# Optimization experiments

Measured on AMD Instinct MI355X. Metric: run time of the kernel, lower is better.

## Reference

```python
import jax, jax.numpy as jnp
import numpy as np

B, C, HID, H, W_ = 16, 2048, 256, 32, 32

def setup_inputs() -> dict:
    key = jax.random.key(0)
    k1, k2, k3 = jax.random.split(key, 3)
    return {
        "query_features": jax.random.normal(k1, (B, C, H, W_), dtype=jnp.float32),
        "prompt_features": jax.random.normal(k2, (B, C, H, W_), dtype=jnp.float32),
        "W": jax.random.normal(k3, (HID, C), dtype=jnp.float32) * 0.02,
        "b": jnp.zeros((HID,), dtype=jnp.float32),
    }

def reference(query_features, prompt_features, W, b):
    Bq, Cc, Hh, Ww = query_features.shape
    HW = Hh * Ww
    # 1x1 conv == channel matmul
    Q = jnp.einsum('oc,bchw->bohw', W, query_features) + b[None, :, None, None]
    K = jnp.einsum('oc,bchw->bohw', W, prompt_features) + b[None, :, None, None]
    Qf = Q.reshape(Bq, -1, HW)          # (b, hid, HW1)
    Kf = K.reshape(Bq, -1, HW)          # (b, hid, HW2)
    Vf = prompt_features.reshape(Bq, Cc, HW)  # (b, C, HW2)
    scores = jnp.einsum('bcq,bck->bqk', Qf, Kf)   # (b, HW1, HW2)
    A = jax.nn.softmax(scores, axis=-1)
    aligned = jnp.einsum('bqk,bck->bcq', A, Vf).reshape(Bq, Cc, Hh, Ww)
    # fusion_policy == 'cat'
    return jnp.concatenate([query_features, aligned], axis=1)
```

## Files before the change

### kernel.cpp

```cpp
#include <hip/hip_runtime.h>

#define NB   16
#define NC   2048
#define NHID 256
#define NHW  1024

using half4_t  = __attribute__((ext_vector_type(4))) _Float16;
using half8_t  = __attribute__((ext_vector_type(8))) _Float16;
using float4_t = __attribute__((ext_vector_type(4))) float;

#define OUT_BATCH_BYTES ((size_t)(4096u * 1024u) * 4u)

__device__ __forceinline__ void async_load16(const void* g, void* l) {
    __builtin_amdgcn_global_load_lds((__attribute__((address_space(1))) void*)g,
                                     (__attribute__((address_space(3))) void*)l, 16, 0, 0);
}

__device__ __forceinline__ void stage_async(const _Float16* __restrict__ src, size_t stride_h,
                                            _Float16* __restrict__ lds, int t) {
    #pragma unroll
    for (int i = 0; i < 4; ++i) {
        const int o   = i * 4096 + t * 16;
        const int row = o >> 7;
        const int s   = ((o >> 4) & 7) ^ (row & 7);
        const _Float16* g = src + (size_t)row * stride_h + s * 8;
        async_load16(g, (char*)lds + o);
    }
}

__device__ __forceinline__ half8_t frag_read(const _Float16* __restrict__ lds, int row, int kk, int quad) {
    const int s = (kk * 4 + quad) ^ (row & 7);
    return *(const half8_t*)((const char*)lds + row * 128 + s * 16);
}

#define ACC_INIT(acc) \
    _Pragma("unroll") for (int i_ = 0; i_ < 4; ++i_) \
    _Pragma("unroll") for (int j_ = 0; j_ < 4; ++j_) \
    _Pragma("unroll") for (int r_ = 0; r_ < 4; ++r_) acc[i_][j_][r_] = 0.f;

__device__ __forceinline__ void gemm_f16(const _Float16* __restrict__ A, size_t lda,
                                         const _Float16* __restrict__ B, size_t ldb,
                                         int K, _Float16* __restrict__ As, _Float16* __restrict__ Bs,
                                         float4_t acc[4][4]) {
    const int t = threadIdx.x;
    const int l = t & 63, quad = l >> 4, l15 = l & 15;
    const int w = t >> 6;
    const int wr = (w >> 1) * 64, wc = (w & 1) * 64;
    for (int k0 = 0; k0 < K; k0 += 64) {
        stage_async(A + k0, lda, As, t);
        stage_async(B + k0, ldb, Bs, t);
        __syncthreads();
        #pragma unroll
        for (int kk = 0; kk < 2; ++kk) {
            half8_t af[4], bf[4];
            #pragma unroll
            for (int i = 0; i < 4; ++i) af[i] = frag_read(As, wr + i * 16 + l15, kk, quad);
            #pragma unroll
            for (int j = 0; j < 4; ++j) bf[j] = frag_read(Bs, wc + j * 16 + l15, kk, quad);
            #pragma unroll
            for (int i = 0; i < 4; ++i)
                #pragma unroll
                for (int j = 0; j < 4; ++j)
                    acc[i][j] = __builtin_amdgcn_mfma_f32_16x16x32_f16(af[i], bf[j], acc[i][j], 0, 0, 0);
        }
        __syncthreads();
    }
}

__global__ __launch_bounds__(256) void prep_kernel(
    const float* __restrict__ qf, const float* __restrict__ pf,
    _Float16* __restrict__ qT, float* __restrict__ out) {
    __shared__ _Float16 tile[64][72];
    const int z = blockIdx.z, which = z >> 4, b = z & 15;
    const int c0 = blockIdx.y * 64, h0 = blockIdx.x * 64;
    const float* X = (which ? pf : qf) + (size_t)b * NC * NHW;
    _Float16* T = which ? (_Float16*)((char*)out + (size_t)b * OUT_BATCH_BYTES + (4u << 20))
                        : (qT + (size_t)b * NHW * NC);
    const int t = threadIdx.x;
    const int row = t >> 2, seg = t & 3;
    const float* src = X + (size_t)(c0 + row) * NHW + h0 + seg * 16;
    float4 v[4];
    #pragma unroll
    for (int i = 0; i < 4; ++i) v[i] = *(const float4*)(src + i * 4);
    half8_t h[2];
    #pragma unroll
    for (int i = 0; i < 2; ++i) {
        #pragma unroll
        for (int e = 0; e < 4; ++e) {
            h[i][e]     = (_Float16)((&v[2 * i].x)[e]);
            h[i][4 + e] = (_Float16)((&v[2 * i + 1].x)[e]);
        }
        *(half8_t*)&tile[row][seg * 16 + i * 8] = h[i];
    }
    if (which) {
        _Float16* vd = (_Float16*)((char*)out + (size_t)b * OUT_BATCH_BYTES)
                       + (size_t)(c0 + row) * NHW + h0 + seg * 16;
        *(half8_t*)vd = h[0];
        *(half8_t*)(vd + 8) = h[1];
    }
    __syncthreads();
    const int hr = t >> 2;
    half8_t o[2];
    #pragma unroll
    for (int i = 0; i < 2; ++i)
        #pragma unroll
        for (int e = 0; e < 8; ++e) o[i][e] = tile[seg * 16 + i * 8 + e][hr];
    _Float16* od = T + (size_t)(h0 + hr) * NC + c0 + seg * 16;
    *(half8_t*)od = o[0];
    *(half8_t*)(od + 8) = o[1];
}

__global__ __launch_bounds__(256) void wcvt_kernel(const float* __restrict__ W, _Float16* __restrict__ W16) {
    const int idx = (blockIdx.x * 256 + threadIdx.x) * 8;
    float4 a = *(const float4*)(W + idx);
    float4 c = *(const float4*)(W + idx + 4);
    half8_t h;
    h[0] = (_Float16)a.x; h[1] = (_Float16)a.y; h[2] = (_Float16)a.z; h[3] = (_Float16)a.w;
    h[4] = (_Float16)c.x; h[5] = (_Float16)c.y; h[6] = (_Float16)c.z; h[7] = (_Float16)c.w;
    *(half8_t*)(W16 + idx) = h;
}

__global__ __launch_bounds__(256) void proj16_kernel(
    const _Float16* __restrict__ qT, const float* __restrict__ out_scratch,
    const _Float16* __restrict__ W16, const float* __restrict__ bias,
    _Float16* __restrict__ Q16, _Float16* __restrict__ K16) {
    __shared__ __attribute__((aligned(16))) _Float16 As[8192];
    __shared__ __attribute__((aligned(16))) _Float16 Bs[8192];
    const int z = blockIdx.z, which = z >> 4, b = z & 15;
    const _Float16* X = which
        ? (const _Float16*)((const char*)out_scratch + (size_t)b * OUT_BATCH_BYTES + (4u << 20))
        : (qT + (size_t)b * NHW * NC);
    _Float16* O = (which ? K16 : Q16) + (size_t)b * NHW * NHID;
    const int m0 = blockIdx.y * 128, n0 = blockIdx.x * 128;
    float4_t acc[4][4];
    ACC_INIT(acc)
    gemm_f16(X + (size_t)m0 * NC, NC, W16 + (size_t)n0 * NC, NC, NC, As, Bs, acc);
    const int t = threadIdx.x, l = t & 63, quad = l >> 4, l15 = l & 15, w = t >> 6;
    const int wr = (w >> 1) * 64, wc = (w & 1) * 64;
    #pragma unroll
    for (int j = 0; j < 4; ++j) {
        const float bv = bias[n0 + wc + j * 16 + l15];
        #pragma unroll
        for (int i = 0; i < 4; ++i)
            #pragma unroll
            for (int r = 0; r < 4; ++r) {
                int hw  = m0 + wr + i * 16 + quad * 4 + r;
                int hid = n0 + wc + j * 16 + l15;
                O[(size_t)hw * NHID + hid] = (_Float16)(acc[i][j][r] + bv);
            }
    }
}

__global__ __launch_bounds__(256) void scores16_kernel(
    const _Float16* __restrict__ Q16, const _Float16* __restrict__ K16, float* __restrict__ S) {
    __shared__ __attribute__((aligned(16))) _Float16 As[8192];
    __shared__ __attribute__((aligned(16))) _Float16 Bs[8192];
    const int b = blockIdx.z;
    const int m0 = blockIdx.y * 128, n0 = blockIdx.x * 128;
    float* Sb = S + (size_t)b * NHW * NHW;
    float4_t acc[4][4];
    ACC_INIT(acc)
    gemm_f16(Q16 + (size_t)b * NHW * NHID + (size_t)m0 * NHID, NHID,
             K16 + (size_t)b * NHW * NHID + (size_t)n0 * NHID, NHID, NHID, As, Bs, acc);
    const int t = threadIdx.x, l = t & 63, quad = l >> 4, l15 = l & 15, w = t >> 6;
    const int wr = (w >> 1) * 64, wc = (w & 1) * 64;
    #pragma unroll
    for (int i = 0; i < 4; ++i)
        #pragma unroll
        for (int j = 0; j < 4; ++j)
            #pragma unroll
            for (int r = 0; r < 4; ++r) {
                int q1 = m0 + wr + i * 16 + quad * 4 + r;
                int q2 = n0 + wc + j * 16 + l15;
                Sb[(size_t)q1 * NHW + q2] = acc[i][j][r];
            }
}

__global__ __launch_bounds__(256) void softmax_kernel(float* __restrict__ S) {
    const int t = threadIdx.x, wave = t >> 6, lane = t & 63;
    float* row = S + ((size_t)blockIdx.x * 4 + wave) * NHW;
    float4 v[4];
    float mx = -1e30f;
    #pragma unroll
    for (int j = 0; j < 4; ++j) {
        v[j] = *(const float4*)(row + (lane << 2) + (j << 8));
        mx = fmaxf(mx, fmaxf(fmaxf(v[j].x, v[j].y), fmaxf(v[j].z, v[j].w)));
    }
    #pragma unroll
    for (int off = 32; off >= 1; off >>= 1) mx = fmaxf(mx, __shfl_xor(mx, off, 64));
    float s = 0.f;
    #pragma unroll
    for (int j = 0; j < 4; ++j) {
        v[j].x = __expf(v[j].x - mx); v[j].y = __expf(v[j].y - mx);
        v[j].z = __expf(v[j].z - mx); v[j].w = __expf(v[j].w - mx);
        s += v[j].x + v[j].y + v[j].z + v[j].w;
    }
    #pragma unroll
    for (int off = 32; off >= 1; off >>= 1) s += __shfl_xor(s, off, 64);
    const float inv = 1.0f / s;
    __syncthreads();
    _Float16* o = (_Float16*)row;
    #pragma unroll
    for (int j = 0; j < 4; ++j) {
        half4_t h;
        h[0] = (_Float16)(v[j].x * inv); h[1] = (_Float16)(v[j].y * inv);
        h[2] = (_Float16)(v[j].z * inv); h[3] = (_Float16)(v[j].w * inv);
        *(half4_t*)(o + (lane << 2) + (j << 8)) = h;
    }
}

__global__ __launch_bounds__(256) void av16_kernel(
    const float* __restrict__ S, float* __restrict__ out) {
    __shared__ __attribute__((aligned(16))) _Float16 As[8192];
    __shared__ __attribute__((aligned(16))) _Float16 Bs[8192];
    const int b = blockIdx.z;
    const _Float16* Vb  = (const _Float16*)((const char*)out + (size_t)b * OUT_BATCH_BYTES);
    const _Float16* A16 = (const _Float16*)(S + (size_t)b * NHW * NHW);
    float* Ob = out + (size_t)b * (2 * NC) * NHW + (size_t)NC * NHW;
    const int m0 = blockIdx.y * 128;
    const int n0 = blockIdx.x * 128;
    float4_t acc[4][4];
    ACC_INIT(acc)
    gemm_f16(Vb + (size_t)m0 * NHW, NHW, A16 + (size_t)n0 * 2048, 2048, NHW, As, Bs, acc);
    const int t = threadIdx.x, l = t & 63, quad = l >> 4, l15 = l & 15, w = t >> 6;
    const int wr = (w >> 1) * 64, wc = (w & 1) * 64;
    #pragma unroll
    for (int i = 0; i < 4; ++i)
        #pragma unroll
        for (int j = 0; j < 4; ++j)
            #pragma unroll
            for (int r = 0; r < 4; ++r) {
                int c = m0 + wr + i * 16 + quad * 4 + r;
                int q = n0 + wc + j * 16 + l15;
                Ob[(size_t)c * NHW + q] = acc[i][j][r];
            }
}

__global__ __launch_bounds__(256) void copy_kernel(const uint4* __restrict__ qf,
                                                   uint4* __restrict__ out) {
    int idx = blockIdx.x * 256 + threadIdx.x;
    int b = idx >> 19;
    int r = idx & 0x7FFFF;
    out[((size_t)b << 20) + r] = qf[idx];
}

extern "C" void kernel_launch(void* const* d_in, const int* in_sizes, int n_in,
                              void* d_out, int out_size, void* d_ws, size_t ws_size,
                              hipStream_t stream) {
    const float* qf   = (const float*)d_in[0];
    const float* pf   = (const float*)d_in[1];
    const float* Wm   = (const float*)d_in[2];
    const float* bias = (const float*)d_in[3];
    float* out = (float*)d_out;

    _Float16* qT  = (_Float16*)d_ws;
    float*    S   = (float*)d_ws;
    _Float16* Q16 = (_Float16*)((char*)d_ws + ((size_t)64 << 20));
    _Float16* K16 = (_Float16*)((char*)d_ws + ((size_t)72 << 20));
    _Float16* W16 = (_Float16*)((char*)out + ((size_t)8 << 20));

    prep_kernel<<<dim3(16, 32, 32), 256, 0, stream>>>(qf, pf, qT, out);
    wcvt_kernel<<<256, 256, 0, stream>>>(Wm, W16);
    proj16_kernel<<<dim3(2, 8, 32), 256, 0, stream>>>(qT, out, W16, bias, Q16, K16);
    scores16_kernel<<<dim3(8, 8, 16), 256, 0, stream>>>(Q16, K16, S);
    softmax_kernel<<<NB * 256, 256, 0, stream>>>(S);
    av16_kernel<<<dim3(8, 16, 16), 256, 0, stream>>>(S, out);
    copy_kernel<<<32768, 256, 0, stream>>>((const uint4*)qf, (uint4*)out);
}
```

Measured before the change: 692.6 us.

## Fuse fp32 transpose-convert into projection GEMM and remap blocks per XCD

Removes the separate transpose/convert prep kernel: the projection GEMM now reads fp32 query/prompt features directly, converts and transposes them into LDS, and computes all 256 hidden outputs per block with 64-row tiles. While doing so it writes the second half of the query passthrough, so the final copy kernel only copies the first half. V conversion becomes a simple elementwise kernel. Scores and AV kernels remap block IDs so that each XCD works on the same batches, improving L2 locality. The trade-off is uncoalesced-ish strided fp32 loads with no async staging in the projection, and smaller grids (512 blocks).

```diff
diff --git a/kernel.cpp b/kernel.cpp
--- a/kernel.cpp
+++ b/kernel.cpp
@@ -16,10 +16,11 @@
                                      (__attribute__((address_space(3))) void*)l, 16, 0, 0);
 }
 
+template <int NROWS>
 __device__ __forceinline__ void stage_async(const _Float16* __restrict__ src, size_t stride_h,
                                             _Float16* __restrict__ lds, int t) {
     #pragma unroll
-    for (int i = 0; i < 4; ++i) {
+    for (int i = 0; i < NROWS / 32; ++i) {
         const int o   = i * 4096 + t * 16;
         const int row = o >> 7;
         const int s   = ((o >> 4) & 7) ^ (row & 7);
@@ -47,8 +48,8 @@
     const int w = t >> 6;
     const int wr = (w >> 1) * 64, wc = (w & 1) * 64;
     for (int k0 = 0; k0 < K; k0 += 64) {
-        stage_async(A + k0, lda, As, t);
-        stage_async(B + k0, ldb, Bs, t);
+        stage_async<128>(A + k0, lda, As, t);
+        stage_async<128>(B + k0, ldb, Bs, t);
         __syncthreads();
         #pragma unroll
         for (int kk = 0; kk < 2; ++kk) {
@@ -67,47 +68,19 @@
     }
 }
 
-__global__ __launch_bounds__(256) void prep_kernel(
-    const float* __restrict__ qf, const float* __restrict__ pf,
-    _Float16* __restrict__ qT, float* __restrict__ out) {
-    __shared__ _Float16 tile[64][72];
-    const int z = blockIdx.z, which = z >> 4, b = z & 15;
-    const int c0 = blockIdx.y * 64, h0 = blockIdx.x * 64;
-    const float* X = (which ? pf : qf) + (size_t)b * NC * NHW;
-    _Float16* T = which ? (_Float16*)((char*)out + (size_t)b * OUT_BATCH_BYTES + (4u << 20))
-                        : (qT + (size_t)b * NHW * NC);
-    const int t = threadIdx.x;
-    const int row = t >> 2, seg = t & 3;
-    const float* src = X + (size_t)(c0 + row) * NHW + h0 + seg * 16;
-    float4 v[4];
-    #pragma unroll
-    for (int i = 0; i < 4; ++i) v[i] = *(const float4*)(src + i * 4);
-    half8_t h[2];
-    #pragma unroll
-    for (int i = 0; i < 2; ++i) {
-        #pragma unroll
-        for (int e = 0; e < 4; ++e) {
-            h[i][e]     = (_Float16)((&v[2 * i].x)[e]);
-            h[i][4 + e] = (_Float16)((&v[2 * i + 1].x)[e]);
-        }
-        *(half8_t*)&tile[row][seg * 16 + i * 8] = h[i];
-    }
-    if (which) {
-        _Float16* vd = (_Float16*)((char*)out + (size_t)b * OUT_BATCH_BYTES)
-                       + (size_t)(c0 + row) * NHW + h0 + seg * 16;
-        *(half8_t*)vd = h[0];
-        *(half8_t*)(vd + 8) = h[1];
-    }
-    __syncthreads();
-    const int hr = t >> 2;
-    half8_t o[2];
-    #pragma unroll
-    for (int i = 0; i < 2; ++i)
-        #pragma unroll
-        for (int e = 0; e < 8; ++e) o[i][e] = tile[seg * 16 + i * 8 + e][hr];
-    _Float16* od = T + (size_t)(h0 + hr) * NC + c0 + seg * 16;
-    *(half8_t*)od = o[0];
-    *(half8_t*)(od + 8) = o[1];
+__global__ __launch_bounds__(256) void prep_v_kernel(const float* __restrict__ pf,
+                                                     float* __restrict__ out) {
+    const int idx = blockIdx.x * 256 + threadIdx.x;
+    const int b = idx >> 18;
+    const int r = idx & 0x3FFFF;
+    const float* src = pf + ((size_t)b << 21) + (size_t)r * 8;
+    float4 a = *(const float4*)src;
+    float4 c = *(const float4*)(src + 4);
+    half8_t h;
+    h[0] = (_Float16)a.x; h[1] = (_Float16)a.y; h[2] = (_Float16)a.z; h[3] = (_Float16)a.w;
+    h[4] = (_Float16)c.x; h[5] = (_Float16)c.y; h[6] = (_Float16)c.z; h[7] = (_Float16)c.w;
+    _Float16* dst = (_Float16*)((char*)out + (size_t)b * OUT_BATCH_BYTES) + (size_t)r * 8;
+    *(half8_t*)dst = h;
 }
 
 __global__ __launch_bounds__(256) void wcvt_kernel(const float* __restrict__ W, _Float16* __restrict__ W16) {
@@ -121,32 +94,75 @@
 }
 
 __global__ __launch_bounds__(256) void proj16_kernel(
-    const _Float16* __restrict__ qT, const float* __restrict__ out_scratch,
+    const float* __restrict__ qf, const float* __restrict__ pf,
     const _Float16* __restrict__ W16, const float* __restrict__ bias,
-    _Float16* __restrict__ Q16, _Float16* __restrict__ K16) {
-    __shared__ __attribute__((aligned(16))) _Float16 As[8192];
-    __shared__ __attribute__((aligned(16))) _Float16 Bs[8192];
+    _Float16* __restrict__ Q16, _Float16* __restrict__ K16,
+    float* __restrict__ out) {
+    __shared__ __attribute__((aligned(16))) _Float16 As[64 * 72];
+    __shared__ __attribute__((aligned(16))) _Float16 Bs[256 * 64];
     const int z = blockIdx.z, which = z >> 4, b = z & 15;
-    const _Float16* X = which
-        ? (const _Float16*)((const char*)out_scratch + (size_t)b * OUT_BATCH_BYTES + (4u << 20))
-        : (qT + (size_t)b * NHW * NC);
+    const float* X = (which ? pf : qf) + (size_t)b * NC * NHW;
+    float* passq = (float*)((char*)out + (size_t)b * OUT_BATCH_BYTES);
     _Float16* O = (which ? K16 : Q16) + (size_t)b * NHW * NHID;
-    const int m0 = blockIdx.y * 128, n0 = blockIdx.x * 128;
+    const int m0 = blockIdx.x * 64;
+    const int t = threadIdx.x;
+    const int l = t & 63, quad = l >> 4, l15 = l & 15;
+    const int w = t >> 6;
+    const int wc = w * 64;
+    const int j = t & 15;
+    const int g = t >> 4;
+
     float4_t acc[4][4];
     ACC_INIT(acc)
-    gemm_f16(X + (size_t)m0 * NC, NC, W16 + (size_t)n0 * NC, NC, NC, As, Bs, acc);
-    const int t = threadIdx.x, l = t & 63, quad = l >> 4, l15 = l & 15, w = t >> 6;
-    const int wr = (w >> 1) * 64, wc = (w & 1) * 64;
-    #pragma unroll
-    for (int j = 0; j < 4; ++j) {
-        const float bv = bias[n0 + wc + j * 16 + l15];
+
+    for (int k0 = 0; k0 < NC; k0 += 64) {
+        float4 xr[4];
+        #pragma unroll
+        for (int r = 0; r < 4; ++r)
+            xr[r] = *(const float4*)(X + (size_t)(k0 + g * 4 + r) * NHW + m0 + j * 4);
+        if (which == 0 && k0 >= 1024) {
+            #pragma unroll
+            for (int r = 0; r < 4; ++r)
+                *(float4*)(passq + (size_t)(k0 + g * 4 + r) * NHW + m0 + j * 4) = xr[r];
+        }
+        #pragma unroll
+        for (int e = 0; e < 4; ++e) {
+            half4_t h;
+            h[0] = (_Float16)((&xr[0].x)[e]);
+            h[1] = (_Float16)((&xr[1].x)[e]);
+            h[2] = (_Float16)((&xr[2].x)[e]);
+            h[3] = (_Float16)((&xr[3].x)[e]);
+            *(half4_t*)(As + (j * 4 + e) * 72 + g * 4) = h;
+        }
+        stage_async<256>(W16 + k0, NC, Bs, t);
+        __syncthreads();
+        #pragma unroll
+        for (int kk = 0; kk < 2; ++kk) {
+            half8_t af[4], bf[4];
+            #pragma unroll
+            for (int i = 0; i < 4; ++i)
+                af[i] = *(const half8_t*)(As + (i * 16 + l15) * 72 + kk * 32 + quad * 8);
+            #pragma unroll
+            for (int jj = 0; jj < 4; ++jj)
+                bf[jj] = frag_read(Bs, wc + jj * 16 + l15, kk, quad);
+            #pragma unroll
+            for (int i = 0; i < 4; ++i)
+                #pragma unroll
+                for (int jj = 0; jj < 4; ++jj)
+                    acc[i][jj] = __builtin_amdgcn_mfma_f32_16x16x32_f16(af[i], bf[jj], acc[i][jj], 0, 0, 0);
+        }
+        __syncthreads();
+    }
+    #pragma unroll
+    for (int jj = 0; jj < 4; ++jj) {
+        const float bv = bias[wc + jj * 16 + l15];
         #pragma unroll
         for (int i = 0; i < 4; ++i)
             #pragma unroll
             for (int r = 0; r < 4; ++r) {
-                int hw  = m0 + wr + i * 16 + quad * 4 + r;
-                int hid = n0 + wc + j * 16 + l15;
-                O[(size_t)hw * NHID + hid] = (_Float16)(acc[i][j][r] + bv);
+                int hw  = m0 + i * 16 + quad * 4 + r;
+                int hid = wc + jj * 16 + l15;
+                O[(size_t)hw * NHID + hid] = (_Float16)(acc[i][jj][r] + bv);
             }
     }
 }
@@ -155,8 +171,10 @@
     const _Float16* __restrict__ Q16, const _Float16* __restrict__ K16, float* __restrict__ S) {
     __shared__ __attribute__((aligned(16))) _Float16 As[8192];
     __shared__ __attribute__((aligned(16))) _Float16 Bs[8192];
-    const int b = blockIdx.z;
-    const int m0 = blockIdx.y * 128, n0 = blockIdx.x * 128;
+    const int oid = blockIdx.x + blockIdx.y * 8 + blockIdx.z * 64;
+    const int xcd = oid & 7, half = (oid >> 9) & 1, r = (oid >> 3) & 63;
+    const int b = xcd * 2 + half;
+    const int m0 = (r >> 3) * 128, n0 = (r & 7) * 128;
     float* Sb = S + (size_t)b * NHW * NHW;
     float4_t acc[4][4];
     ACC_INIT(acc)
@@ -169,10 +187,10 @@
         #pragma unroll
         for (int j = 0; j < 4; ++j)
             #pragma unroll
-            for (int r = 0; r < 4; ++r) {
-                int q1 = m0 + wr + i * 16 + quad * 4 + r;
+            for (int rr = 0; rr < 4; ++rr) {
+                int q1 = m0 + wr + i * 16 + quad * 4 + rr;
                 int q2 = n0 + wc + j * 16 + l15;
-                Sb[(size_t)q1 * NHW + q2] = acc[i][j][r];
+                Sb[(size_t)q1 * NHW + q2] = acc[i][j][rr];
             }
 }
 
@@ -213,12 +231,14 @@
     const float* __restrict__ S, float* __restrict__ out) {
     __shared__ __attribute__((aligned(16))) _Float16 As[8192];
     __shared__ __attribute__((aligned(16))) _Float16 Bs[8192];
-    const int b = blockIdx.z;
+    const int oid = blockIdx.x + blockIdx.y * 8 + blockIdx.z * 128;
+    const int xcd = oid & 7, half = (oid >> 10) & 1, r = (oid >> 3) & 127;
+    const int b = xcd * 2 + half;
+    const int m0 = (r >> 3) * 128;
+    const int n0 = (r & 7) * 128;
     const _Float16* Vb  = (const _Float16*)((const char*)out + (size_t)b * OUT_BATCH_BYTES);
     const _Float16* A16 = (const _Float16*)(S + (size_t)b * NHW * NHW);
     float* Ob = out + (size_t)b * (2 * NC) * NHW + (size_t)NC * NHW;
-    const int m0 = blockIdx.y * 128;
-    const int n0 = blockIdx.x * 128;
     float4_t acc[4][4];
     ACC_INIT(acc)
     gemm_f16(Vb + (size_t)m0 * NHW, NHW, A16 + (size_t)n0 * 2048, 2048, NHW, As, Bs, acc);
@@ -229,19 +249,19 @@
         #pragma unroll
         for (int j = 0; j < 4; ++j)
             #pragma unroll
-            for (int r = 0; r < 4; ++r) {
-                int c = m0 + wr + i * 16 + quad * 4 + r;
+            for (int rr = 0; rr < 4; ++rr) {
+                int c = m0 + wr + i * 16 + quad * 4 + rr;
                 int q = n0 + wc + j * 16 + l15;
-                Ob[(size_t)c * NHW + q] = acc[i][j][r];
+                Ob[(size_t)c * NHW + q] = acc[i][j][rr];
             }
 }
 
-__global__ __launch_bounds__(256) void copy_kernel(const uint4* __restrict__ qf,
-                                                   uint4* __restrict__ out) {
-    int idx = blockIdx.x * 256 + threadIdx.x;
-    int b = idx >> 19;
-    int r = idx & 0x7FFFF;
-    out[((size_t)b << 20) + r] = qf[idx];
+__global__ __launch_bounds__(256) void copy2_kernel(const uint4* __restrict__ qf,
+                                                    uint4* __restrict__ out) {
+    const int idx = blockIdx.x * 256 + threadIdx.x;
+    const int b = idx >> 18;
+    const int r = idx & 0x3FFFF;
+    out[((size_t)b << 20) + r] = qf[((size_t)b << 19) + r];
 }
 
 extern "C" void kernel_launch(void* const* d_in, const int* in_sizes, int n_in,
@@ -253,17 +273,16 @@
     const float* bias = (const float*)d_in[3];
     float* out = (float*)d_out;
 
-    _Float16* qT  = (_Float16*)d_ws;
     float*    S   = (float*)d_ws;
     _Float16* Q16 = (_Float16*)((char*)d_ws + ((size_t)64 << 20));
     _Float16* K16 = (_Float16*)((char*)d_ws + ((size_t)72 << 20));
     _Float16* W16 = (_Float16*)((char*)out + ((size_t)8 << 20));
 
-    prep_kernel<<<dim3(16, 32, 32), 256, 0, stream>>>(qf, pf, qT, out);
     wcvt_kernel<<<256, 256, 0, stream>>>(Wm, W16);
-    proj16_kernel<<<dim3(2, 8, 32), 256, 0, stream>>>(qT, out, W16, bias, Q16, K16);
+    prep_v_kernel<<<16384, 256, 0, stream>>>(pf, out);
+    proj16_kernel<<<dim3(16, 1, 32), 256, 0, stream>>>(qf, pf, W16, bias, Q16, K16, out);
     scores16_kernel<<<dim3(8, 8, 16), 256, 0, stream>>>(Q16, K16, S);
     softmax_kernel<<<NB * 256, 256, 0, stream>>>(S);
     av16_kernel<<<dim3(8, 16, 16), 256, 0, stream>>>(S, out);
-    copy_kernel<<<32768, 256, 0, stream>>>((const uint4*)qf, (uint4*)out);
-}
+    copy2_kernel<<<16384, 256, 0, stream>>>((const uint4*)qf, (uint4*)out);
+}
```

New measurement: 652.3 us. 5.8% less time.
